# Kernel tuning notes

Hardware: AMD Instinct MI355X
Metric: run time of the kernel (lower is better)

The kernel has to match this reference:

```python
import jax, jax.numpy as jnp
import numpy as np

VOCAB, EMBED, HEADS, MAXSEQ = 32000, 1024, 16, 2048
HEAD_DIM = EMBED // HEADS


def setup_inputs() -> dict:
    key = jax.random.key(0)
    ks = jax.random.split(key, 7)
    idx = jax.random.randint(ks[0], (2, 2048), 0, VOCAB)
    # token embedding initialized with eye_ in the original; use identity-like table
    emb = jnp.eye(VOCAB, EMBED, dtype=jnp.float32)
    std = 0.02
    wq = jax.random.normal(ks[1], (EMBED, EMBED), jnp.float32) * std
    wk = jax.random.normal(ks[2], (EMBED, EMBED), jnp.float32) * std
    wv = jax.random.normal(ks[3], (EMBED, EMBED), jnp.float32) * std
    wo = jax.random.normal(ks[4], (EMBED, EMBED), jnp.float32) * std
    wfc = jax.random.normal(ks[5], (VOCAB, EMBED), jnp.float32) * std
    return {"idx": idx, "emb": emb, "wq": wq, "wk": wk, "wv": wv, "wo": wo, "wfc": wfc}


def reference(idx, emb, wq, wk, wv, wo, wfc):
    B, T = idx.shape
    x = emb[idx]  # [B,T,E]
    # projections: torch Linear computes x @ W.T
    def split_heads(y):
        return y.reshape(B, T, HEADS, HEAD_DIM).transpose(0, 2, 1, 3)  # [B,H,T,D]
    q = split_heads(x @ wq.T)
    k = split_heads(x @ wk.T)
    v = split_heads(x @ wv.T)
    scores = jnp.einsum('bhtd,bhsd->bhts', q, k) * (HEAD_DIM ** -0.5)
    mask = jnp.tril(jnp.ones((T, T), dtype=bool))
    scores = jnp.where(mask, scores, -jnp.inf)
    attn = jax.nn.softmax(scores, axis=-1)
    out = jnp.einsum('bhts,bhsd->bhtd', attn, v)  # [B,H,T,D]
    out = out.transpose(0, 2, 1, 3).reshape(B, T, EMBED)
    attn_out = out @ wo.T
    x = x + attn_out  # residual
    logits = x @ wfc.T  # [B,T,V]
    return logits
```

## Files before the change

kernel.cpp:

```cpp
#include <hip/hip_runtime.h>
#include <hip/hip_bf16.h>
#include <stdint.h>

#define VOCAB 32000
#define EMBED 1024
#define HEADS 16
#define SEQ   2048
#define BATCH 2
#define HD    64

typedef __attribute__((ext_vector_type(8))) __bf16 bf16x8;
typedef __attribute__((ext_vector_type(4))) __bf16 bf16x4;
typedef __attribute__((ext_vector_type(4))) float f32x4;
typedef __attribute__((ext_vector_type(8))) unsigned short u16x8;

__device__ __forceinline__ void gload16(const void* g, void* l) {
  __builtin_amdgcn_global_load_lds((const __attribute__((address_space(1))) void*)g,
                                   (__attribute__((address_space(3))) void*)l,
                                   16, 0, 0);
}

__global__ __launch_bounds__(256) void k_embed(const int* __restrict__ idx,
                                               const float* __restrict__ emb,
                                               float* __restrict__ xf,
                                               __bf16* __restrict__ xb) {
  const int row = blockIdx.x;
  const int t = threadIdx.x;
  const int src = idx[row];
  float4 v = reinterpret_cast<const float4*>(emb + (size_t)src * EMBED)[t];
  reinterpret_cast<float4*>(xf + (size_t)row * EMBED)[t] = v;
  bf16x4 b;
  b[0] = (__bf16)v.x; b[1] = (__bf16)v.y; b[2] = (__bf16)v.z; b[3] = (__bf16)v.w;
  reinterpret_cast<bf16x4*>(xb + (size_t)row * EMBED)[t] = b;
}

__global__ __launch_bounds__(256) void k_f2b(const float* __restrict__ in,
                                             __bf16* __restrict__ out, int n4) {
  int i = blockIdx.x * 256 + threadIdx.x;
  if (i >= n4) return;
  float4 v = reinterpret_cast<const float4*>(in)[i];
  bf16x4 b;
  b[0] = (__bf16)v.x; b[1] = (__bf16)v.y; b[2] = (__bf16)v.z; b[3] = (__bf16)v.w;
  reinterpret_cast<bf16x4*>(out)[i] = b;
}

template<int MODE>
__global__ __launch_bounds__(256) void k_gemm(const __bf16* __restrict__ A,
                                              const __bf16* __restrict__ Bt,
                                              int M, int N, int K,
                                              float* __restrict__ Cf,
                                              __bf16* __restrict__ Cb,
                                              const float* __restrict__ resid) {
  __shared__ __bf16 As[128 * 32];
  __shared__ __bf16 Bs[128 * 32];
  const int tid = threadIdx.x;
  const int wid = tid >> 6, lane = tid & 63;
  const int m0 = blockIdx.x * 128, n0 = blockIdx.y * 128;
  const int wr = wid >> 1, wc = wid & 1;

  const int arow = tid >> 2, acol = (tid & 3) * 8;
  const __bf16* ga0 = A + (size_t)(m0 + arow) * K + acol;
  const __bf16* ga1 = A + (size_t)(m0 + arow + 64) * K + acol;
  const __bf16* gb0 = Bt + (size_t)(n0 + arow) * K + acol;
  const __bf16* gb1 = Bt + (size_t)(n0 + arow + 64) * K + acol;
  __bf16* lA0 = As + wid * 512;
  __bf16* lA1 = As + wid * 512 + 2048;
  __bf16* lB0 = Bs + wid * 512;
  __bf16* lB1 = Bs + wid * 512 + 2048;

  f32x4 acc[4][4] = {};
  const int lr = lane & 15;
  const int kchunk = (lane >> 4) * 8;

  for (int k0 = 0; k0 < K; k0 += 32) {
    gload16(ga0 + k0, lA0);
    gload16(ga1 + k0, lA1);
    gload16(gb0 + k0, lB0);
    gload16(gb1 + k0, lB1);
    __syncthreads();
    bf16x8 a[4], b[4];
#pragma unroll
    for (int i = 0; i < 4; ++i) {
      a[i] = *reinterpret_cast<const bf16x8*>(&As[(wr * 64 + i * 16 + lr) * 32 + kchunk]);
      b[i] = *reinterpret_cast<const bf16x8*>(&Bs[(wc * 64 + i * 16 + lr) * 32 + kchunk]);
    }
#pragma unroll
    for (int i = 0; i < 4; ++i)
#pragma unroll
      for (int j = 0; j < 4; ++j)
        acc[i][j] = __builtin_amdgcn_mfma_f32_16x16x32_bf16(a[i], b[j], acc[i][j], 0, 0, 0);
    __syncthreads();
  }

  const int r0 = (lane >> 4) * 4;
#pragma unroll
  for (int i = 0; i < 4; ++i)
#pragma unroll
    for (int j = 0; j < 4; ++j)
#pragma unroll
      for (int r = 0; r < 4; ++r) {
        const int row = m0 + wr * 64 + i * 16 + r0 + r;
        const int col = n0 + wc * 64 + j * 16 + lr;
        const size_t o = (size_t)row * N + col;
        if constexpr (MODE == 0)      Cf[o] = acc[i][j][r];
        else if constexpr (MODE == 1) Cb[o] = (__bf16)acc[i][j][r];
        else                          Cb[o] = (__bf16)(acc[i][j][r] + resid[o]);
      }
}

__global__ __launch_bounds__(256) void k_attn(const __bf16* __restrict__ qb,
                                              const __bf16* __restrict__ kb,
                                              const __bf16* __restrict__ vb,
                                              __bf16* __restrict__ ctx) {
  __shared__ __bf16 Ks[64 * 64];
  __shared__ __bf16 Vt[64 * 64];
  __shared__ __bf16 Ps[4][16 * 64];

  const int tid = threadIdx.x, wid = tid >> 6, lane = tid & 63;
  const int bq = blockIdx.x;
  const int bh = blockIdx.y;
  const int b = bh >> 4, h = bh & 15;
  const int q0 = bq * 64;

  const size_t qoff = (size_t)(b * SEQ + q0 + wid * 16 + (lane & 15)) * EMBED + h * HD;
  const bf16x8 qf0 = *reinterpret_cast<const bf16x8*>(qb + qoff + (lane >> 4) * 8);
  const bf16x8 qf1 = *reinterpret_cast<const bf16x8*>(qb + qoff + 32 + (lane >> 4) * 8);

  const int krow = tid >> 3;
  const int kcs = (tid & 7) ^ (krow & 7);
  const __bf16* kg = kb + (size_t)(b * SEQ + krow) * EMBED + h * HD + kcs * 8;
  __bf16* lK0 = Ks + wid * 512;
  __bf16* lK1 = Ks + wid * 512 + 2048;

  const int vkv = (tid & 31) * 2;
  const int vd0 = (tid >> 5) * 8;
  const __bf16* vg = vb + (size_t)(b * SEQ + vkv) * EMBED + h * HD + vd0;

  f32x4 o[4] = {};
  float mrow[4] = {-1e30f, -1e30f, -1e30f, -1e30f};
  float lsum[4] = {0.f, 0.f, 0.f, 0.f};

  char* const pbase = (char*)&Ps[wid][0];
  const char* const ksb = (const char*)Ks;
  const char* const vtb = (const char*)Vt;

  const int ntiles = bq + 1;
  for (int t = 0; t < ntiles; ++t) {
    const size_t kvo = (size_t)t * 64 * EMBED;
    gload16(kg + kvo, lK0);
    gload16(kg + kvo + (size_t)32 * EMBED, lK1);
    u16x8 v0 = *reinterpret_cast<const u16x8*>(vg + kvo);
    u16x8 v1 = *reinterpret_cast<const u16x8*>(vg + kvo + EMBED);
#pragma unroll
    for (int j = 0; j < 8; ++j) {
      uint32_t val = (uint32_t)v0[j] | ((uint32_t)v1[j] << 16);
      *(uint32_t*)((char*)Vt + (vd0 + j) * 128 + ((vkv * 2) ^ (j << 4))) = val;
    }
    __syncthreads();

    f32x4 s[4];
#pragma unroll
    for (int nb = 0; nb < 4; ++nb) {
      const int n = nb * 16 + (lane & 15);
      const int c0 = (lane >> 4) ^ (n & 7);
      const int c1 = ((lane >> 4) + 4) ^ (n & 7);
      bf16x8 kf0 = *reinterpret_cast<const bf16x8*>(ksb + n * 128 + c0 * 16);
      bf16x8 kf1 = *reinterpret_cast<const bf16x8*>(ksb + n * 128 + c1 * 16);
      f32x4 z = {};
      z = __builtin_amdgcn_mfma_f32_16x16x32_bf16(qf0, kf0, z, 0, 0, 0);
      z = __builtin_amdgcn_mfma_f32_16x16x32_bf16(qf1, kf1, z, 0, 0, 0);
      s[nb] = z;
    }

    const int kvb = t * 64;
    const int qrow0 = q0 + wid * 16 + (lane >> 4) * 4;
#pragma unroll
    for (int nb = 0; nb < 4; ++nb) {
      const int kcol = kvb + nb * 16 + (lane & 15);
#pragma unroll
      for (int r = 0; r < 4; ++r) {
        float x = s[nb][r] * 0.125f;
        s[nb][r] = (kcol <= qrow0 + r) ? x : -1e30f;
      }
    }

    float pmax[4], alpha[4], rsum[4];
#pragma unroll
    for (int r = 0; r < 4; ++r)
      pmax[r] = fmaxf(fmaxf(s[0][r], s[1][r]), fmaxf(s[2][r], s[3][r]));
#pragma unroll
    for (int off = 1; off < 16; off <<= 1)
#pragma unroll
      for (int r = 0; r < 4; ++r)
        pmax[r] = fmaxf(pmax[r], __shfl_xor(pmax[r], off, 64));
#pragma unroll
    for (int r = 0; r < 4; ++r) {
      float mn = fmaxf(mrow[r], pmax[r]);
      alpha[r] = __expf(mrow[r] - mn);
      mrow[r] = mn;
      rsum[r] = 0.f;
    }
#pragma unroll
    for (int nb = 0; nb < 4; ++nb)
#pragma unroll
      for (int r = 0; r < 4; ++r) {
        float p = __expf(s[nb][r] - mrow[r]);
        s[nb][r] = p;
        rsum[r] += p;
      }
#pragma unroll
    for (int off = 1; off < 16; off <<= 1)
#pragma unroll
      for (int r = 0; r < 4; ++r)
        rsum[r] += __shfl_xor(rsum[r], off, 64);
#pragma unroll
    for (int r = 0; r < 4; ++r)
      lsum[r] = lsum[r] * alpha[r] + rsum[r];
#pragma unroll
    for (int nb = 0; nb < 4; ++nb)
#pragma unroll
      for (int r = 0; r < 4; ++r)
        o[nb][r] *= alpha[r];

#pragma unroll
    for (int nb = 0; nb < 4; ++nb)
#pragma unroll
      for (int r = 0; r < 4; ++r) {
        const int pr = (lane >> 4) * 4 + r;
        const int pc = nb * 16 + (lane & 15);
        *(__bf16*)(pbase + pr * 128 + ((pc * 2) ^ ((pr & 7) << 4))) = (__bf16)s[nb][r];
      }
    const int ar = lane & 15;
    const int aswz = (ar & 7) << 4;
    bf16x8 pf0 = *reinterpret_cast<const bf16x8*>(pbase + ar * 128 + (((lane >> 4) * 16) ^ aswz));
    bf16x8 pf1 = *reinterpret_cast<const bf16x8*>(pbase + ar * 128 + ((64 + (lane >> 4) * 16) ^ aswz));

#pragma unroll
    for (int nb = 0; nb < 4; ++nb) {
      const int n = nb * 16 + (lane & 15);
      const int vswz = (n & 7) << 4;
      bf16x8 vf0 = *reinterpret_cast<const bf16x8*>(vtb + n * 128 + (((lane >> 4) * 16) ^ vswz));
      bf16x8 vf1 = *reinterpret_cast<const bf16x8*>(vtb + n * 128 + ((64 + (lane >> 4) * 16) ^ vswz));
      o[nb] = __builtin_amdgcn_mfma_f32_16x16x32_bf16(pf0, vf0, o[nb], 0, 0, 0);
      o[nb] = __builtin_amdgcn_mfma_f32_16x16x32_bf16(pf1, vf1, o[nb], 0, 0, 0);
    }
    __syncthreads();
  }

  const int orow = q0 + wid * 16 + (lane >> 4) * 4;
#pragma unroll
  for (int nb = 0; nb < 4; ++nb)
#pragma unroll
    for (int r = 0; r < 4; ++r) {
      const float v = o[nb][r] / lsum[r];
      ctx[(size_t)(b * SEQ + orow + r) * EMBED + h * HD + nb * 16 + (lane & 15)] = (__bf16)v;
    }
}

extern "C" void kernel_launch(void* const* d_in, const int* in_sizes, int n_in,
                              void* d_out, int out_size, void* d_ws, size_t ws_size,
                              hipStream_t stream) {
  const int*   idx = (const int*)d_in[0];
  const float* emb = (const float*)d_in[1];
  const float* wq  = (const float*)d_in[2];
  const float* wk  = (const float*)d_in[3];
  const float* wv  = (const float*)d_in[4];
  const float* wo  = (const float*)d_in[5];
  const float* wfc = (const float*)d_in[6];
  float* out = (float*)d_out;

  char* ws = (char*)d_ws;
  float*  xf  = (float*)(ws);
  __bf16* xb  = (__bf16*)(ws + 16777216);
  __bf16* qbf = (__bf16*)(ws + 25165824);
  __bf16* kbf = (__bf16*)(ws + 33554432);
  __bf16* vbf = (__bf16*)(ws + 41943040);
  __bf16* cbf = (__bf16*)(ws + 50331648);
  __bf16* x2b = (__bf16*)(ws + 58720256);
  __bf16* wqb = (__bf16*)(ws + 67108864);
  __bf16* wkb = (__bf16*)(ws + 69206016);
  __bf16* wvb = (__bf16*)(ws + 71303168);
  __bf16* wob = (__bf16*)(ws + 73400320);
  __bf16* wfb = (__bf16*)(ws + 75497472);

  k_embed<<<dim3(4096), dim3(256), 0, stream>>>(idx, emb, xf, xb);
  k_f2b<<<dim3(1024), dim3(256), 0, stream>>>(wq, wqb, 262144);
  k_f2b<<<dim3(1024), dim3(256), 0, stream>>>(wk, wkb, 262144);
  k_f2b<<<dim3(1024), dim3(256), 0, stream>>>(wv, wvb, 262144);
  k_f2b<<<dim3(1024), dim3(256), 0, stream>>>(wo, wob, 262144);
  k_f2b<<<dim3(32000), dim3(256), 0, stream>>>(wfc, wfb, 8192000);

  k_gemm<1><<<dim3(32, 8), dim3(256), 0, stream>>>(xb, wqb, 4096, 1024, 1024, nullptr, qbf, nullptr);
  k_gemm<1><<<dim3(32, 8), dim3(256), 0, stream>>>(xb, wkb, 4096, 1024, 1024, nullptr, kbf, nullptr);
  k_gemm<1><<<dim3(32, 8), dim3(256), 0, stream>>>(xb, wvb, 4096, 1024, 1024, nullptr, vbf, nullptr);

  k_attn<<<dim3(32, 32), dim3(256), 0, stream>>>(qbf, kbf, vbf, cbf);

  k_gemm<2><<<dim3(32, 8), dim3(256), 0, stream>>>(cbf, wob, 4096, 1024, 1024, nullptr, x2b, xf);

  k_gemm<0><<<dim3(32, 250), dim3(256), 0, stream>>>(x2b, wfb, 4096, 32000, 1024, out, nullptr, nullptr);
}
```

Before: 1.252 ms.

## Add 256x256 pipelined GEMM for logits and fuse QKV projections

Introduces a 512-thread GEMM kernel with 256x256 tiles, double-buffered direct-to-LDS loads, interleaved MFMA quarters with priority hints, and XCD-aware block remapping, used for the large vocab projection. Also concatenates wq/wk/wv into one weight buffer so Q, K and V come from a single GEMM, with attention reading strided rows. The aim is higher data reuse and MFMA utilisation on the dominant logits GEMM and fewer launches for QKV. The large tile uses 128 KB LDS and many accumulator registers, which limits occupancy.

```diff
diff --git a/kernel.cpp b/kernel.cpp
--- a/kernel.cpp
+++ b/kernel.cpp
@@ -19,6 +19,7 @@
                                    (__attribute__((address_space(3))) void*)l,
                                    16, 0, 0);
 }
+#define BAR() asm volatile("s_barrier" ::: "memory")
 
 __global__ __launch_bounds__(256) void k_embed(const int* __restrict__ idx,
                                                const float* __restrict__ emb,
@@ -102,6 +103,149 @@
         const int row = m0 + wr * 64 + i * 16 + r0 + r;
         const int col = n0 + wc * 64 + j * 16 + lr;
         const size_t o = (size_t)row * N + col;
+        if constexpr (MODE == 1) Cb[o] = (__bf16)acc[i][j][r];
+        else                     Cb[o] = (__bf16)(acc[i][j][r] + resid[o]);
+      }
+}
+
+template<int MODE>
+__global__ __launch_bounds__(512, 2) void k_gemm256(const __bf16* __restrict__ A,
+                                                    const __bf16* __restrict__ Bt,
+                                                    int M, int N, int K,
+                                                    float* __restrict__ Cf,
+                                                    __bf16* __restrict__ Cb,
+                                                    const float* __restrict__ resid,
+                                                    int grid_m) {
+  __shared__ __bf16 lds[65536];
+  char* const sb = (char*)lds;
+
+  const int tid = threadIdx.x;
+  const int wid = tid >> 6, lane = tid & 63;
+  const int wm = wid >> 2, wn = wid & 3;
+  const int lr = lane & 15, lk = lane >> 4;
+
+  const int nwg = gridDim.x;
+  const int orig = blockIdx.x;
+  const int xcd = orig & 7, qq = nwg >> 3, rr = nwg & 7;
+  const int wg = (xcd < rr ? xcd * (qq + 1) : rr * (qq + 1) + (xcd - rr) * qq) + (orig >> 3);
+  const int m0 = (wg % grid_m) << 8;
+  const int n0 = (wg / grid_m) << 8;
+  const int nt = K >> 6;
+
+  const int scc = (tid & 7) ^ (((tid >> 5) & 1) << 1);
+  const int sArow = tid >> 3;
+  const int sBrow = ((tid >> 8) & 1) * 64 + ((tid >> 3) & 31);
+  const __bf16* aG[2][2];
+  const __bf16* bG[2][2];
+#pragma unroll
+  for (int s = 0; s < 2; ++s) {
+#pragma unroll
+    for (int h = 0; h < 2; ++h) {
+      aG[s][h] = A + (size_t)(m0 + s * 128 + h * 64 + sArow) * K + scc * 8;
+      bG[s][h] = Bt + (size_t)(n0 + s * 128 + sBrow + h * 32) * K + scc * 8;
+    }
+  }
+  const int aDstW = wid * 1024;
+  const int bDstW = (wm * 64 + wn * 8) * 128;
+
+  auto stageA = [&](int t, int hi) {
+    const int bb = (t & 1) << 16;
+    const size_t ko = (size_t)(t << 6);
+#pragma unroll
+    for (int s = 0; s < 2; ++s)
+      gload16(aG[s][hi] + ko, sb + bb + s * 16384 + hi * 8192 + aDstW);
+  };
+  auto stageB = [&](int t, int hiq) {
+    const int bb = (t & 1) << 16;
+    const size_t ko = (size_t)(t << 6);
+#pragma unroll
+    for (int s = 0; s < 2; ++s)
+      gload16(bG[s][hiq] + ko, sb + bb + 32768 + s * 16384 + hiq * 4096 + bDstW);
+  };
+
+  const int axor = ((lr >> 2) & 1) << 5;
+  const int aBase = wm * 16384;
+  const int bBase = 32768 + (wn >> 1) * 16384 + (wn & 1) * 8192;
+
+  f32x4 acc[8][4] = {};
+  bf16x8 Ar[4][2], Blo[2][2], Bhi[2][2];
+
+  auto ldA = [&](int bb, int ih) {
+    const char* p = sb + bb + aBase;
+#pragma unroll
+    for (int ii = 0; ii < 4; ++ii) {
+      const int ro = (ih * 64 + ii * 16 + lr) * 128;
+#pragma unroll
+      for (int kk = 0; kk < 2; ++kk)
+        Ar[ii][kk] = *reinterpret_cast<const bf16x8*>(p + ro + kk * 64 + ((lk * 16) ^ axor));
+    }
+  };
+  auto ldB = [&](int bb, bf16x8 (&B)[2][2], int jh) {
+    const char* p = sb + bb + bBase;
+#pragma unroll
+    for (int jj = 0; jj < 2; ++jj) {
+      const int ro = ((jh * 2 + jj) * 16 + lr) * 128;
+#pragma unroll
+      for (int kk = 0; kk < 2; ++kk)
+        B[jj][kk] = *reinterpret_cast<const bf16x8*>(p + ro + kk * 64 + ((lk * 16) ^ axor));
+    }
+  };
+  auto mmaQ = [&](int i0, int j0, bf16x8 (&B)[2][2]) {
+    __builtin_amdgcn_s_setprio(1);
+#pragma unroll
+    for (int ii = 0; ii < 4; ++ii)
+#pragma unroll
+      for (int jj = 0; jj < 2; ++jj)
+#pragma unroll
+        for (int kk = 0; kk < 2; ++kk)
+          acc[i0 + ii][j0 + jj] = __builtin_amdgcn_mfma_f32_16x16x32_bf16(
+              Ar[ii][kk], B[jj][kk], acc[i0 + ii][j0 + jj], 0, 0, 0);
+    __builtin_amdgcn_s_setprio(0);
+  };
+
+  stageA(0, 0); stageB(0, 1); stageA(0, 1); stageB(0, 0);
+  stageA(1, 0); stageB(1, 1);
+  asm volatile("s_waitcnt vmcnt(4)" ::: "memory");
+  __builtin_amdgcn_sched_barrier(0);
+  BAR();
+
+  for (int t = 0; t < nt; ++t) {
+    const int bb = (t & 1) << 16;
+    ldA(bb, 0); ldB(bb, Blo, 0);
+    if (t + 1 < nt) stageA(t + 1, 1);
+    BAR();
+    mmaQ(0, 0, Blo);
+    BAR();
+    ldB(bb, Bhi, 1);
+    if (t + 1 < nt) stageB(t + 1, 0);
+    BAR();
+    mmaQ(0, 2, Bhi);
+    BAR();
+    ldA(bb, 1);
+    if (t + 2 < nt) stageA(t + 2, 0);
+    BAR();
+    mmaQ(4, 2, Bhi);
+    BAR();
+    if (t + 2 < nt) stageB(t + 2, 1);
+    if (t < nt - 1) {
+      if (t + 2 < nt) { asm volatile("s_waitcnt vmcnt(4)" ::: "memory"); }
+      else            { asm volatile("s_waitcnt vmcnt(0)" ::: "memory"); }
+      __builtin_amdgcn_sched_barrier(0);
+    }
+    BAR();
+    mmaQ(4, 0, Blo);
+    BAR();
+  }
+
+  const int rbase = m0 + wm * 128 + lk * 4;
+  const int cbase = n0 + wn * 64 + lr;
+#pragma unroll
+  for (int i = 0; i < 8; ++i)
+#pragma unroll
+    for (int j = 0; j < 4; ++j)
+#pragma unroll
+      for (int r = 0; r < 4; ++r) {
+        const size_t o = (size_t)(rbase + i * 16 + r) * N + (cbase + j * 16);
         if constexpr (MODE == 0)      Cf[o] = acc[i][j][r];
         else if constexpr (MODE == 1) Cb[o] = (__bf16)acc[i][j][r];
         else                          Cb[o] = (__bf16)(acc[i][j][r] + resid[o]);
@@ -111,7 +255,7 @@
 __global__ __launch_bounds__(256) void k_attn(const __bf16* __restrict__ qb,
                                               const __bf16* __restrict__ kb,
                                               const __bf16* __restrict__ vb,
-                                              __bf16* __restrict__ ctx) {
+                                              __bf16* __restrict__ ctx, int ld) {
   __shared__ __bf16 Ks[64 * 64];
   __shared__ __bf16 Vt[64 * 64];
   __shared__ __bf16 Ps[4][16 * 64];
@@ -122,19 +266,19 @@
   const int b = bh >> 4, h = bh & 15;
   const int q0 = bq * 64;
 
-  const size_t qoff = (size_t)(b * SEQ + q0 + wid * 16 + (lane & 15)) * EMBED + h * HD;
+  const size_t qoff = (size_t)(b * SEQ + q0 + wid * 16 + (lane & 15)) * ld + h * HD;
   const bf16x8 qf0 = *reinterpret_cast<const bf16x8*>(qb + qoff + (lane >> 4) * 8);
   const bf16x8 qf1 = *reinterpret_cast<const bf16x8*>(qb + qoff + 32 + (lane >> 4) * 8);
 
   const int krow = tid >> 3;
   const int kcs = (tid & 7) ^ (krow & 7);
-  const __bf16* kg = kb + (size_t)(b * SEQ + krow) * EMBED + h * HD + kcs * 8;
+  const __bf16* kg = kb + (size_t)(b * SEQ + krow) * ld + h * HD + kcs * 8;
   __bf16* lK0 = Ks + wid * 512;
   __bf16* lK1 = Ks + wid * 512 + 2048;
 
   const int vkv = (tid & 31) * 2;
   const int vd0 = (tid >> 5) * 8;
-  const __bf16* vg = vb + (size_t)(b * SEQ + vkv) * EMBED + h * HD + vd0;
+  const __bf16* vg = vb + (size_t)(b * SEQ + vkv) * ld + h * HD + vd0;
 
   f32x4 o[4] = {};
   float mrow[4] = {-1e30f, -1e30f, -1e30f, -1e30f};
@@ -146,11 +290,11 @@
 
   const int ntiles = bq + 1;
   for (int t = 0; t < ntiles; ++t) {
-    const size_t kvo = (size_t)t * 64 * EMBED;
+    const size_t kvo = (size_t)t * 64 * ld;
     gload16(kg + kvo, lK0);
-    gload16(kg + kvo + (size_t)32 * EMBED, lK1);
+    gload16(kg + kvo + (size_t)32 * ld, lK1);
     u16x8 v0 = *reinterpret_cast<const u16x8*>(vg + kvo);
-    u16x8 v1 = *reinterpret_cast<const u16x8*>(vg + kvo + EMBED);
+    u16x8 v1 = *reinterpret_cast<const u16x8*>(vg + kvo + ld);
 #pragma unroll
     for (int j = 0; j < 8; ++j) {
       uint32_t val = (uint32_t)v0[j] | ((uint32_t)v1[j] << 16);
@@ -272,31 +416,25 @@
   char* ws = (char*)d_ws;
   float*  xf  = (float*)(ws);
   __bf16* xb  = (__bf16*)(ws + 16777216);
-  __bf16* qbf = (__bf16*)(ws + 25165824);
-  __bf16* kbf = (__bf16*)(ws + 33554432);
-  __bf16* vbf = (__bf16*)(ws + 41943040);
+  __bf16* qkv = (__bf16*)(ws + 25165824);
   __bf16* cbf = (__bf16*)(ws + 50331648);
   __bf16* x2b = (__bf16*)(ws + 58720256);
   __bf16* wqb = (__bf16*)(ws + 67108864);
-  __bf16* wkb = (__bf16*)(ws + 69206016);
-  __bf16* wvb = (__bf16*)(ws + 71303168);
   __bf16* wob = (__bf16*)(ws + 73400320);
   __bf16* wfb = (__bf16*)(ws + 75497472);
 
   k_embed<<<dim3(4096), dim3(256), 0, stream>>>(idx, emb, xf, xb);
   k_f2b<<<dim3(1024), dim3(256), 0, stream>>>(wq, wqb, 262144);
-  k_f2b<<<dim3(1024), dim3(256), 0, stream>>>(wk, wkb, 262144);
-  k_f2b<<<dim3(1024), dim3(256), 0, stream>>>(wv, wvb, 262144);
+  k_f2b<<<dim3(1024), dim3(256), 0, stream>>>(wk, wqb + 1048576, 262144);
+  k_f2b<<<dim3(1024), dim3(256), 0, stream>>>(wv, wqb + 2097152, 262144);
   k_f2b<<<dim3(1024), dim3(256), 0, stream>>>(wo, wob, 262144);
   k_f2b<<<dim3(32000), dim3(256), 0, stream>>>(wfc, wfb, 8192000);
 
-  k_gemm<1><<<dim3(32, 8), dim3(256), 0, stream>>>(xb, wqb, 4096, 1024, 1024, nullptr, qbf, nullptr);
-  k_gemm<1><<<dim3(32, 8), dim3(256), 0, stream>>>(xb, wkb, 4096, 1024, 1024, nullptr, kbf, nullptr);
-  k_gemm<1><<<dim3(32, 8), dim3(256), 0, stream>>>(xb, wvb, 4096, 1024, 1024, nullptr, vbf, nullptr);
-
-  k_attn<<<dim3(32, 32), dim3(256), 0, stream>>>(qbf, kbf, vbf, cbf);
+  k_gemm<1><<<dim3(32, 24), dim3(256), 0, stream>>>(xb, wqb, 4096, 3072, 1024, nullptr, qkv, nullptr);
+
+  k_attn<<<dim3(32, 32), dim3(256), 0, stream>>>(qkv, qkv + 1024, qkv + 2048, cbf, 3072);
 
   k_gemm<2><<<dim3(32, 8), dim3(256), 0, stream>>>(cbf, wob, 4096, 1024, 1024, nullptr, x2b, xf);
 
-  k_gemm<0><<<dim3(32, 250), dim3(256), 0, stream>>>(x2b, wfb, 4096, 32000, 1024, out, nullptr, nullptr);
-}
+  k_gemm256<0><<<dim3(2000), dim3(512), 0, stream>>>(x2b, wfb, 4096, 32000, 1024, out, nullptr, nullptr, 16);
+}
```

After: 1.142 ms. 8.8% less time.
